# Kernel optimization log

Hardware: AMD Instinct MI355X
Metric: run time of the kernel (lower is better)

The kernel has to match this reference:

```python
import jax, jax.numpy as jnp
import numpy as np
from jax import lax

B, L = 128, 256
DW, DC = 100, 30
H = 400          # hidden_size (bidirectional total)
HD = H // 2      # per-direction hidden
NT = 18          # tag vocab size (BIOES)
VW, VC = 400000, 50000


def setup_inputs():
    key = jax.random.key(0)
    ks = iter(jax.random.split(key, 64))
    rn = lambda shape, s=0.1: jax.random.normal(next(ks), shape, jnp.float32) * s
    inp = {
        "words": jax.random.randint(next(ks), (B, L), 0, VW),
        "cap_words": jax.random.randint(next(ks), (B, L), 0, VC),
        "seq_len": jax.random.randint(next(ks), (B,), L // 2, L + 1),
        "target": jax.random.randint(next(ks), (B, L), 0, NT),
        "word_emb": rn((VW, DW)),
        "char_emb": rn((VC, DC)),
    }
    for l, din in ((0, DW + DC), (1, H)):
        for d in ("f", "b"):
            inp[f"W_ih_l{l}{d}"] = rn((4 * HD, din))
            inp[f"W_hh_l{l}{d}"] = rn((4 * HD, HD))
            inp[f"b_ih_l{l}{d}"] = rn((4 * HD,))
            inp[f"b_hh_l{l}{d}"] = rn((4 * HD,))
    inp["Wf"], inp["bf"] = rn((NT, HD)), jnp.zeros((NT,), jnp.float32)
    inp["Wb"], inp["bb"] = rn((NT, HD)), jnp.zeros((NT,), jnp.float32)
    inp["trans"] = rn((NT, NT))
    return inp


def _lstm_dir(x, W_ih, W_hh, b_ih, b_hh):
    # x: [B, L, D] -> hidden states [B, L, HD]; torch gate order i, f, g, o
    Bsz = x.shape[0]
    def step(carry, xt):
        h, c = carry
        g = xt @ W_ih.T + b_ih + h @ W_hh.T + b_hh
        i, f, gg, o = jnp.split(g, 4, axis=-1)
        c = jax.nn.sigmoid(f) * c + jax.nn.sigmoid(i) * jnp.tanh(gg)
        h = jax.nn.sigmoid(o) * jnp.tanh(c)
        return (h, c), h
    init = (jnp.zeros((Bsz, HD), x.dtype), jnp.zeros((Bsz, HD), x.dtype))
    _, hs = lax.scan(step, init, jnp.swapaxes(x, 0, 1))
    return jnp.swapaxes(hs, 0, 1)


def _rev(x, seq_len):
    # reverse each sequence within its true length (padding stays in place),
    # emulating pack_padded_sequence semantics for the backward direction
    t = jnp.arange(x.shape[1])[None, :]
    idx = jnp.where(t < seq_len[:, None], seq_len[:, None] - 1 - t, t)
    return jnp.take_along_axis(x, idx[:, :, None], axis=1)


def _crf_nll(logits, tags, mask, trans):
    # normalizer: forward algorithm, logsumexp scan over time with mask
    def step(alpha, inp):
        emit, m = inp  # emit: [B, NT], m: [B] bool
        new = jax.nn.logsumexp(alpha[:, :, None] + trans[None] + emit[:, None, :], axis=1)
        return jnp.where(m[:, None], new, alpha), None
    emits = jnp.swapaxes(logits, 0, 1)  # [L, B, NT]
    ms = jnp.swapaxes(mask, 0, 1)
    alpha, _ = lax.scan(step, emits[0], (emits[1:], ms[1:]))
    z = jax.nn.logsumexp(alpha, axis=1)
    # gold path score
    mf = mask.astype(logits.dtype)
    emit_sc = jnp.take_along_axis(logits, tags[:, :, None], axis=2)[:, :, 0]
    gold = jnp.sum(emit_sc * mf, axis=1) + jnp.sum(trans[tags[:, :-1], tags[:, 1:]] * mf[:, 1:], axis=1)
    return z - gold  # per-sample negative log-likelihood, shape [B]


def _model(words, cap_words, seq_len, target, word_emb, char_emb,
           W_ih_l0f, W_hh_l0f, b_ih_l0f, b_hh_l0f, W_ih_l0b, W_hh_l0b, b_ih_l0b, b_hh_l0b,
           W_ih_l1f, W_hh_l1f, b_ih_l1f, b_hh_l1f, W_ih_l1b, W_hh_l1b, b_ih_l1b, b_hh_l1b,
           Wf, bf, Wb, bb, trans):
    mask = jnp.arange(L)[None, :] < seq_len[:, None]  # [B, L] bool
    mf = mask.astype(jnp.float32)[:, :, None]
    x = jnp.concatenate([word_emb[words], char_emb[cap_words]], axis=-1)
    layers = (((W_ih_l0f, W_hh_l0f, b_ih_l0f, b_hh_l0f), (W_ih_l0b, W_hh_l0b, b_ih_l0b, b_hh_l0b)),
              ((W_ih_l1f, W_hh_l1f, b_ih_l1f, b_hh_l1f), (W_ih_l1b, W_hh_l1b, b_ih_l1b, b_hh_l1b)))
    h = x
    for fp, bp in layers:
        fwd = _lstm_dir(h, *fp)
        bwd = _rev(_lstm_dir(_rev(h, seq_len), *bp), seq_len)
        h = jnp.concatenate([fwd, bwd], axis=-1) * mf  # zero padded steps like packed LSTM
    forwards, backwards = h[..., :HD], h[..., HD:]
    logits = forwards @ Wf.T + bf + backwards @ Wb.T + bb
    return _crf_nll(logits, target, mask, trans)


def reference(words, cap_words, seq_len, target, word_emb, char_emb,
              W_ih_l0f, W_hh_l0f, b_ih_l0f, b_hh_l0f, W_ih_l0b, W_hh_l0b, b_ih_l0b, b_hh_l0b,
              W_ih_l1f, W_hh_l1f, b_ih_l1f, b_hh_l1f, W_ih_l1b, W_hh_l1b, b_ih_l1b, b_hh_l1b,
              Wf, bf, Wb, bb, trans):
    return _model(words, cap_words, seq_len, target, word_emb, char_emb,
                  W_ih_l0f, W_hh_l0f, b_ih_l0f, b_hh_l0f, W_ih_l0b, W_hh_l0b, b_ih_l0b, b_hh_l0b,
                  W_ih_l1f, W_hh_l1f, b_ih_l1f, b_hh_l1f, W_ih_l1b, W_hh_l1b, b_ih_l1b, b_hh_l1b,
                  Wf, bf, Wb, bb, trans)
```

## Files before the change

### kernel.cpp

```cpp
#include <hip/hip_runtime.h>
#include <math.h>

#define B_   128
#define L_   256
#define DW_  100
#define DC_  30
#define HD_  200
#define NT_  18
#define SG   4
#define KP0  160
#define KP1  416

typedef _Float16 half8 __attribute__((ext_vector_type(8)));
typedef _Float16 half4 __attribute__((ext_vector_type(4)));
typedef float    f32x4 __attribute__((ext_vector_type(4)));

__device__ __forceinline__ float frcp_(float x) { return __builtin_amdgcn_rcpf(x); }
__device__ __forceinline__ float sigm_(float x) { return frcp_(1.0f + __expf(-x)); }
__device__ __forceinline__ float tanh_(float x) { return 1.0f - 2.0f * frcp_(1.0f + __expf(2.0f * x)); }

__global__ void k_embed(const int* __restrict__ words, const int* __restrict__ caps,
                        const float* __restrict__ wemb, const float* __restrict__ cemb,
                        _Float16* __restrict__ x) {
    int pos = blockIdx.x;
    int w = words[pos], c = caps[pos];
    _Float16* xp = x + (size_t)pos * KP0;
    for (int t = threadIdx.x; t < KP0; t += blockDim.x) {
        float v = 0.f;
        if (t < DW_) v = wemb[(size_t)w * DW_ + t];
        else if (t < DW_ + DC_) v = cemb[(size_t)c * DC_ + (t - DW_)];
        xp[t] = (_Float16)v;
    }
}

__global__ void k_perm_ih16(const float* __restrict__ src, _Float16* __restrict__ dst,
                            int K, int Kpad, int colOff) {
    int i = blockIdx.x * blockDim.x + threadIdx.x;
    if (i >= 800 * Kpad) return;
    int r = i / Kpad, k = i - r * Kpad;
    int jh = r % 200, g = r / 200;
    int col = colOff + (jh << 2) + g;
    dst[(size_t)col * Kpad + k] = (k < K) ? (_Float16)src[(size_t)r * K + k] : (_Float16)0.f;
}

__global__ void k_bias_perm(const float* bi_f, const float* bh_f,
                            const float* bi_b, const float* bh_b, float* bias) {
    int j = blockIdx.x * blockDim.x + threadIdx.x;
    if (j >= 1600) return;
    int dir = j / 800, r = j - dir * 800;
    int col = dir * 800 + ((r % 200) << 2) + (r / 200);
    bias[col] = dir ? (bi_b[r] + bh_b[r]) : (bi_f[r] + bh_f[r]);
}

__global__ void k_wlog(const float* __restrict__ Wf, const float* __restrict__ bfv,
                       const float* __restrict__ Wb, const float* __restrict__ bbv,
                       float* __restrict__ wlog, float* __restrict__ blog) {
    int i = blockIdx.x * blockDim.x + threadIdx.x;
    if (i < NT_ * 400) {
        int t = i / 400, k = i - t * 400;
        wlog[i] = (k < HD_) ? Wf[t * HD_ + k] : Wb[t * HD_ + (k - HD_)];
    }
    if (i < NT_) blog[i] = bfv[i] + bbv[i];
}

__global__ __launch_bounds__(256) void k_gemm16(const _Float16* __restrict__ A,
                                                const _Float16* __restrict__ Bt,
                                                const float* __restrict__ bias,
                                                _Float16* __restrict__ C,
                                                int Kpad) {
    __shared__ __align__(16) _Float16 sA[128 * 40];
    __shared__ __align__(16) _Float16 sB[64 * 40];
    const int tid = threadIdx.x;
    const int w = tid >> 6, l = tid & 63, l15 = l & 15, lq = l >> 4;
    const int m0 = blockIdx.y * 128, n0 = blockIdx.x * 64;
    const int rw = (w >> 1) * 64, cw = (w & 1) * 32;
    f32x4 acc[4][2];
    #pragma unroll
    for (int i = 0; i < 4; i++)
        #pragma unroll
        for (int j = 0; j < 2; j++) acc[i][j] = f32x4{0.f, 0.f, 0.f, 0.f};

    for (int k0 = 0; k0 < Kpad; k0 += 32) {
        {
            int m = tid >> 1, c = (tid & 1) << 4;
            const _Float16* ap = A + (size_t)(m0 + m) * Kpad + k0 + c;
            *(half8*)&sA[m * 40 + c]     = *(const half8*)ap;
            *(half8*)&sA[m * 40 + c + 8] = *(const half8*)(ap + 8);
        }
        {
            int n = tid >> 2, k8 = (tid & 3) << 3;
            *(half8*)&sB[n * 40 + k8] = *(const half8*)&Bt[(size_t)(n0 + n) * Kpad + k0 + k8];
        }
        __syncthreads();
        half8 aF[4], bF[2];
        #pragma unroll
        for (int i = 0; i < 4; i++) aF[i] = *(const half8*)&sA[(rw + i * 16 + l15) * 40 + lq * 8];
        #pragma unroll
        for (int j = 0; j < 2; j++) bF[j] = *(const half8*)&sB[(cw + j * 16 + l15) * 40 + lq * 8];
        #pragma unroll
        for (int i = 0; i < 4; i++)
            #pragma unroll
            for (int j = 0; j < 2; j++)
                acc[i][j] = __builtin_amdgcn_mfma_f32_16x16x32_f16(aF[i], bF[j], acc[i][j], 0, 0, 0);
        __syncthreads();
    }
    #pragma unroll
    for (int j = 0; j < 2; j++) {
        int n = n0 + cw + j * 16 + l15;
        float bv = bias[n];
        #pragma unroll
        for (int i = 0; i < 4; i++) {
            int mrow = m0 + rw + i * 16 + lq * 4;
            #pragma unroll
            for (int r = 0; r < 4; r++)
                C[(size_t)(mrow + r) * 1600 + n] = (_Float16)(acc[i][j][r] + bv);
        }
    }
}

__global__ __launch_bounds__(512, 2) void k_scan6(const _Float16* __restrict__ gates,
                                                  const float* __restrict__ Whh_f,
                                                  const float* __restrict__ Whh_b,
                                                  const int* __restrict__ seq_len,
                                                  _Float16* __restrict__ hout, int ldH) {
    const int dir = blockIdx.x & 1;
    const int b0  = (blockIdx.x >> 1) * SG;
    const int tid = threadIdx.x;
    const int w   = tid >> 6;
    const int l   = tid & 63;
    const int l15 = l & 15;
    const int lq  = l >> 4;

    __shared__ __align__(16) _Float16 hA[2][16 * 232];
    __shared__ __align__(16) _Float16 bEx[2 * 7 * 512];
    __shared__ __align__(16) _Float16 glds[2][3200];
    __shared__ __align__(16) float    gD[8 * 448];
    __shared__ int ssl[SG];

    const float* W = dir ? Whh_b : Whh_f;
    const int nT = (w < 2) ? 7 : 6;
    const int nCell = nT * 16;

    half8 Breg[6][7];
    #pragma unroll
    for (int i = 0; i < 6; i++) {
        int n  = (w * 6 + i) * 16 + l15;
        int jh = n >> 2, g = n & 3;
        const float* Wr = W + (size_t)(g * 200 + jh) * 200;
        #pragma unroll
        for (int kt = 0; kt < 7; kt++) {
            int k0 = kt * 32 + lq * 8;
            half8 f;
            #pragma unroll
            for (int j = 0; j < 8; j++) {
                int k = k0 + j;
                f[j] = (k < 200) ? (_Float16)Wr[k] : (_Float16)0.f;
            }
            Breg[i][kt] = f;
        }
    }
    if (w < 2) {
        int n  = (48 + w) * 16 + l15;
        int jh = n >> 2, g = n & 3;
        const float* Wr = W + (size_t)(g * 200 + jh) * 200;
        for (int kt = 0; kt < 7; kt++) {
            int k0 = kt * 32 + lq * 8;
            half8 f;
            for (int j = 0; j < 8; j++) {
                int k = k0 + j;
                f[j] = (k < 200) ? (_Float16)Wr[k] : (_Float16)0.f;
            }
            *(half8*)&bEx[(w * 7 + kt) * 512 + l * 8] = f;
        }
    }
    for (int i = tid; i < 2 * 16 * 232; i += 512) (&hA[0][0])[i] = (_Float16)0.f;
    if (tid < SG) ssl[tid] = seq_len[b0 + tid];

    const int  v    = tid;
    const bool stv  = v < 400;
    const int  m_st = v / 100;
    const int  u_st = v - m_st * 100;
    const int  sl_st = stv ? seq_len[b0 + m_st] : L_;
    const _Float16* gbase_st = gates + ((size_t)(b0 + m_st) * L_) * 1600 + dir * 800 + u_st * 8;

    const int cA = l;
    const int iA = cA >> 4, qA = (cA >> 2) & 3, mA = cA & 3;
    const int tgA = (iA < 6) ? (w * 6 + iA) : (48 + w);
    const int hcA = tgA * 4 + qA;
    const int cB = l + 64;
    const int iB = cB >> 4, qB = (cB >> 2) & 3, mB = cB & 3;
    const bool vB = cB < nCell;
    const int tgB = (iB < 6) ? (w * 6 + iB) : (48 + w);
    const int hcB = tgB * 4 + qB;
    float csA = 0.f, csB = 0.f;

    if (stv) {
        int rn = dir ? ((sl_st > 0) ? sl_st - 1 : 0) : 0;
        half8 stg = *(const half8*)(gbase_st + (size_t)rn * 1600);
        *(half8*)&glds[0][v * 8] = stg;
    }
    __syncthreads();

    const f32x4 Cz = {0.f, 0.f, 0.f, 0.f};
    for (int t = 0; t < L_; t++) {
        const int p = t & 1;

        half8 stgn;
        const bool doStg = stv && (t + 1 < L_);
        if (doStg) {
            int tn = t + 1;
            int rn = dir ? ((tn < sl_st) ? sl_st - 1 - tn : tn) : tn;
            stgn = *(const half8*)(gbase_st + (size_t)rn * 1600);
        }

        if (t > 0 && stv) {
            int tp = t - 1;
            int b  = m_st;
            int hp = u_st;
            int slb = ssl[b];
            int row = dir ? ((tp < slb) ? slb - 1 - tp : tp) : tp;
            unsigned int val = (tp < slb) ? *(const unsigned int*)&hA[p][b * 232 + 2 * hp] : 0u;
            *(unsigned int*)&hout[((size_t)(b0 + b) * L_ + row) * ldH + dir * HD_ + 2 * hp] = val;
        }

        f32x4 C[7];
        #pragma unroll
        for (int i = 0; i < 7; i++) C[i] = Cz;
        #pragma unroll
        for (int kt = 0; kt < 7; kt++) {
            half8 hF = *(const half8*)&hA[p][l15 * 232 + kt * 32 + lq * 8];
            #pragma unroll
            for (int i = 0; i < 6; i++)
                C[i] = __builtin_amdgcn_mfma_f32_16x16x32_f16(Breg[i][kt], hF, C[i], 0, 0, 0);
            if (w < 2) {
                half8 bF = *(const half8*)&bEx[(w * 7 + kt) * 512 + l * 8];
                C[6] = __builtin_amdgcn_mfma_f32_16x16x32_f16(bF, hF, C[6], 0, 0, 0);
            }
        }

        if (l15 < 4) {
            #pragma unroll
            for (int i = 0; i < 6; i++)
                *(f32x4*)&gD[w * 448 + (i * 16 + lq * 4 + l15) * 4] = C[i];
            if (w < 2)
                *(f32x4*)&gD[w * 448 + (6 * 16 + lq * 4 + l15) * 4] = C[6];
        }

        {
            f32x4 gv = *(const f32x4*)&gD[w * 448 + cA * 4];
            half4 gi4 = *(const half4*)&glds[p][mA * 800 + 4 * hcA];
            float xi = gv[0] + (float)gi4[0];
            float xf = gv[1] + (float)gi4[1];
            float xg = gv[2] + (float)gi4[2];
            float xo = gv[3] + (float)gi4[3];
            float cn = sigm_(xf) * csA + sigm_(xi) * tanh_(xg);
            csA = cn;
            hA[1 - p][mA * 232 + hcA] = (_Float16)(sigm_(xo) * tanh_(cn));
        }
        if (vB) {
            f32x4 gv = *(const f32x4*)&gD[w * 448 + cB * 4];
            half4 gi4 = *(const half4*)&glds[p][mB * 800 + 4 * hcB];
            float xi = gv[0] + (float)gi4[0];
            float xf = gv[1] + (float)gi4[1];
            float xg = gv[2] + (float)gi4[2];
            float xo = gv[3] + (float)gi4[3];
            float cn = sigm_(xf) * csB + sigm_(xi) * tanh_(xg);
            csB = cn;
            hA[1 - p][mB * 232 + hcB] = (_Float16)(sigm_(xo) * tanh_(cn));
        }

        if (doStg) *(half8*)&glds[1 - p][v * 8] = stgn;

        __syncthreads();
    }
    if (stv) {
        int tp = L_ - 1;
        int b  = m_st;
        int hp = u_st;
        int slb = ssl[b];
        int row = dir ? ((tp < slb) ? slb - 1 - tp : tp) : tp;
        unsigned int val = (tp < slb) ? *(const unsigned int*)&hA[0][b * 232 + 2 * hp] : 0u;
        *(unsigned int*)&hout[((size_t)(b0 + b) * L_ + row) * ldH + dir * HD_ + 2 * hp] = val;
    }
}

__global__ __launch_bounds__(256) void k_logits(const _Float16* __restrict__ h1,
                                                const float* __restrict__ wlog,
                                                const float* __restrict__ blog,
                                                float* __restrict__ logits) {
    __shared__ float sh[8][400];
    __shared__ float sw[NT_ * 400];
    int p0 = blockIdx.x * 8;
    for (int i = threadIdx.x; i < 8 * 400; i += 256)
        sh[i / 400][i % 400] = (float)h1[(size_t)p0 * 400 + i];
    for (int i = threadIdx.x; i < NT_ * 400; i += 256) sw[i] = wlog[i];
    __syncthreads();
    if (threadIdx.x < 8 * NT_) {
        int pi = threadIdx.x / NT_, tg = threadIdx.x % NT_;
        float a = blog[tg];
        #pragma unroll 4
        for (int k = 0; k < 400; k++) a += sh[pi][k] * sw[tg * 400 + k];
        logits[((size_t)(p0 + pi)) * NT_ + tg] = a;
    }
}

__global__ __launch_bounds__(64) void k_crf(const float* __restrict__ logits,
                                            const int* __restrict__ target,
                                            const int* __restrict__ seq_len,
                                            const float* __restrict__ trans,
                                            float* __restrict__ out) {
    int b = blockIdx.x, tid = threadIdx.x;
    __shared__ float str[NT_ * NT_];
    __shared__ float alpha[NT_];
    __shared__ float sgold[1];
    for (int i = tid; i < NT_ * NT_; i += 64) str[i] = trans[i];
    int sl = seq_len[b];
    const float* lg = logits + (size_t)b * L_ * NT_;
    const int* tg = target + (size_t)b * L_;
    if (tid < NT_) alpha[tid] = lg[tid];
    float gacc = 0.f;
    for (int t = tid; t < L_; t += 64) {
        if (t < sl) {
            gacc += lg[t * NT_ + tg[t]];
            if (t >= 1) gacc += trans[tg[t - 1] * NT_ + tg[t]];
        }
    }
    #pragma unroll
    for (int off = 32; off; off >>= 1) gacc += __shfl_down(gacc, off);
    if (tid == 0) sgold[0] = gacc;
    __syncthreads();
    for (int t = 1; t < L_; t++) {
        if (t < sl) {
            float vv = 0.f;
            if (tid < NT_) {
                float mx = -1e30f;
                #pragma unroll
                for (int i = 0; i < NT_; i++) mx = fmaxf(mx, alpha[i] + str[i * NT_ + tid]);
                float s = 0.f;
                #pragma unroll
                for (int i = 0; i < NT_; i++) s += __expf(alpha[i] + str[i * NT_ + tid] - mx);
                vv = mx + __logf(s) + lg[t * NT_ + tid];
            }
            __syncthreads();
            if (tid < NT_) alpha[tid] = vv;
            __syncthreads();
        }
    }
    if (tid == 0) {
        float mx = -1e30f;
        for (int i = 0; i < NT_; i++) mx = fmaxf(mx, alpha[i]);
        float s = 0.f;
        for (int i = 0; i < NT_; i++) s += __expf(alpha[i] - mx);
        out[b] = (mx + __logf(s)) - sgold[0];
    }
}

extern "C" void kernel_launch(void* const* d_in, const int* in_sizes, int n_in,
                              void* d_out, int out_size, void* d_ws, size_t ws_size,
                              hipStream_t stream) {
    const int*   words  = (const int*)d_in[0];
    const int*   caps   = (const int*)d_in[1];
    const int*   seq    = (const int*)d_in[2];
    const int*   target = (const int*)d_in[3];
    const float* wemb   = (const float*)d_in[4];
    const float* cemb   = (const float*)d_in[5];
    const float* Wih0f  = (const float*)d_in[6];
    const float* Whh0f  = (const float*)d_in[7];
    const float* bih0f  = (const float*)d_in[8];
    const float* bhh0f  = (const float*)d_in[9];
    const float* Wih0b  = (const float*)d_in[10];
    const float* Whh0b  = (const float*)d_in[11];
    const float* bih0b  = (const float*)d_in[12];
    const float* bhh0b  = (const float*)d_in[13];
    const float* Wih1f  = (const float*)d_in[14];
    const float* Whh1f  = (const float*)d_in[15];
    const float* bih1f  = (const float*)d_in[16];
    const float* bhh1f  = (const float*)d_in[17];
    const float* Wih1b  = (const float*)d_in[18];
    const float* Whh1b  = (const float*)d_in[19];
    const float* bih1b  = (const float*)d_in[20];
    const float* bhh1b  = (const float*)d_in[21];
    const float* Wf     = (const float*)d_in[22];
    const float* bfv    = (const float*)d_in[23];
    const float* Wb     = (const float*)d_in[24];
    const float* bbv    = (const float*)d_in[25];
    const float* trans  = (const float*)d_in[26];

    char* base = (char*)d_ws;
    _Float16* gatesH = (_Float16*)(base + 0);
    _Float16* xbuf   = (_Float16*)(base + 104857600);
    _Float16* h0b    = (_Float16*)(base + 115343360);
    _Float16* h1b    = xbuf;
    float* logitsb   = (float*)(base + 142606336);
    _Float16* wihT0  = (_Float16*)(base + 144965632);
    _Float16* wihT1  = (_Float16*)(base + 145477632);
    float* bias0     = (float*)(base + 146808832);
    float* bias1     = (float*)(base + 146815232);
    float* wlog      = (float*)(base + 146821632);
    float* blog      = (float*)(base + 146850432);

    k_perm_ih16<<<(800 * KP0 + 255) / 256, 256, 0, stream>>>(Wih0f, wihT0, 130, KP0, 0);
    k_perm_ih16<<<(800 * KP0 + 255) / 256, 256, 0, stream>>>(Wih0b, wihT0, 130, KP0, 800);
    k_perm_ih16<<<(800 * KP1 + 255) / 256, 256, 0, stream>>>(Wih1f, wihT1, 400, KP1, 0);
    k_perm_ih16<<<(800 * KP1 + 255) / 256, 256, 0, stream>>>(Wih1b, wihT1, 400, KP1, 800);
    k_bias_perm<<<7, 256, 0, stream>>>(bih0f, bhh0f, bih0b, bhh0b, bias0);
    k_bias_perm<<<7, 256, 0, stream>>>(bih1f, bhh1f, bih1b, bhh1b, bias1);
    k_wlog<<<(NT_ * 400 + 255) / 256, 256, 0, stream>>>(Wf, bfv, Wb, bbv, wlog, blog);

    k_embed<<<B_ * L_, 128, 0, stream>>>(words, caps, wemb, cemb, xbuf);

    hipMemsetAsync(h0b, 0, (size_t)32768 * KP1 * sizeof(_Float16), stream);

    k_gemm16<<<dim3(25, 256), 256, 0, stream>>>(xbuf, wihT0, bias0, gatesH, KP0);
    k_scan6<<<(B_ / SG) * 2, 512, 0, stream>>>(gatesH, Whh0f, Whh0b, seq, h0b, KP1);

    k_gemm16<<<dim3(25, 256), 256, 0, stream>>>(h0b, wihT1, bias1, gatesH, KP1);
    k_scan6<<<(B_ / SG) * 2, 512, 0, stream>>>(gatesH, Whh1f, Whh1b, seq, h1b, 400);

    k_logits<<<(B_ * L_) / 8, 256, 0, stream>>>(h1b, wlog, blog, logitsb);
    k_crf<<<B_, 64, 0, stream>>>(logitsb, target, seq, trans, (float*)d_out);
}
```

Measured before the change: 1.475 ms.

## Prefetch input gates into registers two steps ahead and use lgkm-only barrier

The LSTM scan kernel stops staging the precomputed input-gate slice through a shared-memory double buffer. Each cell thread now loads its own half4 of gate inputs directly from global memory into registers, two timesteps ahead. The per-step __syncthreads is replaced by a barrier that waits only on LDS counters (lgkmcnt), so outstanding global loads no longer stall the serial recurrence. This removes LDS traffic and a full vmcnt wait from every step, at the cost of extra registers and more scattered, smaller global loads.

Result: no change. 1.478 ms (+0.2%).

```diff
diff --git a/kernel.cpp b/kernel.cpp
--- a/kernel.cpp
+++ b/kernel.cpp
@@ -18,6 +18,12 @@
 __device__ __forceinline__ float frcp_(float x) { return __builtin_amdgcn_rcpf(x); }
 __device__ __forceinline__ float sigm_(float x) { return frcp_(1.0f + __expf(-x)); }
 __device__ __forceinline__ float tanh_(float x) { return 1.0f - 2.0f * frcp_(1.0f + __expf(2.0f * x)); }
+
+__device__ __forceinline__ void barrier_lgkm() {
+    asm volatile("s_waitcnt lgkmcnt(0)" ::: "memory");
+    __builtin_amdgcn_s_barrier();
+    asm volatile("" ::: "memory");
+}
 
 __global__ void k_embed(const int* __restrict__ words, const int* __restrict__ caps,
                         const float* __restrict__ wemb, const float* __restrict__ cemb,
@@ -118,7 +124,7 @@
     }
 }
 
-__global__ __launch_bounds__(512, 2) void k_scan6(const _Float16* __restrict__ gates,
+__global__ __launch_bounds__(512, 2) void k_scan7(const _Float16* __restrict__ gates,
                                                   const float* __restrict__ Whh_f,
                                                   const float* __restrict__ Whh_b,
                                                   const int* __restrict__ seq_len,
@@ -133,7 +139,6 @@
 
     __shared__ __align__(16) _Float16 hA[2][16 * 232];
     __shared__ __align__(16) _Float16 bEx[2 * 7 * 512];
-    __shared__ __align__(16) _Float16 glds[2][3200];
     __shared__ __align__(16) float    gD[8 * 448];
     __shared__ int ssl[SG];
 
@@ -180,8 +185,6 @@
     const bool stv  = v < 400;
     const int  m_st = v / 100;
     const int  u_st = v - m_st * 100;
-    const int  sl_st = stv ? seq_len[b0 + m_st] : L_;
-    const _Float16* gbase_st = gates + ((size_t)(b0 + m_st) * L_) * 1600 + dir * 800 + u_st * 8;
 
     const int cA = l;
     const int iA = cA >> 4, qA = (cA >> 2) & 3, mA = cA & 3;
@@ -194,33 +197,36 @@
     const int hcB = tgB * 4 + qB;
     float csA = 0.f, csB = 0.f;
 
-    if (stv) {
-        int rn = dir ? ((sl_st > 0) ? sl_st - 1 : 0) : 0;
-        half8 stg = *(const half8*)(gbase_st + (size_t)rn * 1600);
-        *(half8*)&glds[0][v * 8] = stg;
-    }
     __syncthreads();
+
+    const int slA = ssl[mA];
+    const int slB = ssl[mB];
+    const int slb_st = stv ? ssl[m_st] : 0;
+    const _Float16* gA_base = gates + ((size_t)(b0 + mA) * L_) * 1600 + dir * 800 + 4 * hcA;
+    const _Float16* gB_base = gates + ((size_t)(b0 + mB) * L_) * 1600 + dir * 800 + 4 * hcB;
+    _Float16* hout_base = hout + (size_t)(b0 + m_st) * L_ * ldH + dir * HD_ + 2 * u_st;
+
+    auto rowOf = [&](int t, int sl) -> int {
+        return dir ? ((t < sl) ? sl - 1 - t : t) : t;
+    };
+
+    half4 gA0, gA1, gB0, gB1;
+    gA0 = *(const half4*)(gA_base + (size_t)rowOf(0, slA) * 1600);
+    gA1 = *(const half4*)(gA_base + (size_t)rowOf(1, slA) * 1600);
+    if (vB) {
+        gB0 = *(const half4*)(gB_base + (size_t)rowOf(0, slB) * 1600);
+        gB1 = *(const half4*)(gB_base + (size_t)rowOf(1, slB) * 1600);
+    }
 
     const f32x4 Cz = {0.f, 0.f, 0.f, 0.f};
     for (int t = 0; t < L_; t++) {
         const int p = t & 1;
 
-        half8 stgn;
-        const bool doStg = stv && (t + 1 < L_);
-        if (doStg) {
-            int tn = t + 1;
-            int rn = dir ? ((tn < sl_st) ? sl_st - 1 - tn : tn) : tn;
-            stgn = *(const half8*)(gbase_st + (size_t)rn * 1600);
-        }
-
         if (t > 0 && stv) {
             int tp = t - 1;
-            int b  = m_st;
-            int hp = u_st;
-            int slb = ssl[b];
-            int row = dir ? ((tp < slb) ? slb - 1 - tp : tp) : tp;
-            unsigned int val = (tp < slb) ? *(const unsigned int*)&hA[p][b * 232 + 2 * hp] : 0u;
-            *(unsigned int*)&hout[((size_t)(b0 + b) * L_ + row) * ldH + dir * HD_ + 2 * hp] = val;
+            int row = dir ? ((tp < slb_st) ? slb_st - 1 - tp : tp) : tp;
+            unsigned int val = (tp < slb_st) ? *(const unsigned int*)&hA[p][m_st * 232 + 2 * u_st] : 0u;
+            *(unsigned int*)(hout_base + (size_t)row * ldH) = val;
         }
 
         f32x4 C[7];
@@ -248,39 +254,39 @@
 
         {
             f32x4 gv = *(const f32x4*)&gD[w * 448 + cA * 4];
-            half4 gi4 = *(const half4*)&glds[p][mA * 800 + 4 * hcA];
-            float xi = gv[0] + (float)gi4[0];
-            float xf = gv[1] + (float)gi4[1];
-            float xg = gv[2] + (float)gi4[2];
-            float xo = gv[3] + (float)gi4[3];
+            float xi = gv[0] + (float)gA0[0];
+            float xf = gv[1] + (float)gA0[1];
+            float xg = gv[2] + (float)gA0[2];
+            float xo = gv[3] + (float)gA0[3];
             float cn = sigm_(xf) * csA + sigm_(xi) * tanh_(xg);
             csA = cn;
             hA[1 - p][mA * 232 + hcA] = (_Float16)(sigm_(xo) * tanh_(cn));
         }
         if (vB) {
             f32x4 gv = *(const f32x4*)&gD[w * 448 + cB * 4];
-            half4 gi4 = *(const half4*)&glds[p][mB * 800 + 4 * hcB];
-            float xi = gv[0] + (float)gi4[0];
-            float xf = gv[1] + (float)gi4[1];
-            float xg = gv[2] + (float)gi4[2];
-            float xo = gv[3] + (float)gi4[3];
+            float xi = gv[0] + (float)gB0[0];
+            float xf = gv[1] + (float)gB0[1];
+            float xg = gv[2] + (float)gB0[2];
+            float xo = gv[3] + (float)gB0[3];
             float cn = sigm_(xf) * csB + sigm_(xi) * tanh_(xg);
             csB = cn;
             hA[1 - p][mB * 232 + hcB] = (_Float16)(sigm_(xo) * tanh_(cn));
         }
 
-        if (doStg) *(half8*)&glds[1 - p][v * 8] = stgn;
-
-        __syncthreads();
+        gA0 = gA1;
+        gB0 = gB1;
+        if (t + 2 < L_) {
+            gA1 = *(const half4*)(gA_base + (size_t)rowOf(t + 2, slA) * 1600);
+            if (vB) gB1 = *(const half4*)(gB_base + (size_t)rowOf(t + 2, slB) * 1600);
+        }
+
+        barrier_lgkm();
     }
     if (stv) {
         int tp = L_ - 1;
-        int b  = m_st;
-        int hp = u_st;
-        int slb = ssl[b];
-        int row = dir ? ((tp < slb) ? slb - 1 - tp : tp) : tp;
-        unsigned int val = (tp < slb) ? *(const unsigned int*)&hA[0][b * 232 + 2 * hp] : 0u;
-        *(unsigned int*)&hout[((size_t)(b0 + b) * L_ + row) * ldH + dir * HD_ + 2 * hp] = val;
+        int row = dir ? ((tp < slb_st) ? slb_st - 1 - tp : tp) : tp;
+        unsigned int val = (tp < slb_st) ? *(const unsigned int*)&hA[0][m_st * 232 + 2 * u_st] : 0u;
+        *(unsigned int*)(hout_base + (size_t)row * ldH) = val;
     }
 }
 
@@ -412,10 +418,10 @@
     hipMemsetAsync(h0b, 0, (size_t)32768 * KP1 * sizeof(_Float16), stream);
 
     k_gemm16<<<dim3(25, 256), 256, 0, stream>>>(xbuf, wihT0, bias0, gatesH, KP0);
-    k_scan6<<<(B_ / SG) * 2, 512, 0, stream>>>(gatesH, Whh0f, Whh0b, seq, h0b, KP1);
+    k_scan7<<<(B_ / SG) * 2, 512, 0, stream>>>(gatesH, Whh0f, Whh0b, seq, h0b, KP1);
 
     k_gemm16<<<dim3(25, 256), 256, 0, stream>>>(h0b, wihT1, bias1, gatesH, KP1);
-    k_scan6<<<(B_ / SG) * 2, 512, 0, stream>>>(gatesH, Whh1f, Whh1b, seq, h1b, 400);
+    k_scan7<<<(B_ / SG) * 2, 512, 0, stream>>>(gatesH, Whh1f, Whh1b, seq, h1b, 400);
 
     k_logits<<<(B_ * L_) / 8, 256, 0, stream>>>(h1b, wlog, blog, logitsb);
     k_crf<<<B_, 64, 0, stream>>>(logitsb, target, seq, trans, (float*)d_out);
```
